# Kernel optimization log

Hardware: AMD Instinct MI355X
Metric: run time of the kernel (lower is better)

The kernel has to match this reference:

```python
import jax, jax.numpy as jnp
import numpy as np

NS, NC, T, NB = 32, 16, 64, 512
NSC = NS + NC


def setup_inputs() -> dict:
    key = jax.random.key(0)
    k1, k2, k3, k4, k5 = jax.random.split(key, 5)
    # SPD cost matrices so Quu is invertible (as assumed by the LQR math)
    L = jax.random.normal(k1, (NB, T, NSC, NSC), jnp.float32) * 0.1
    Q = L @ jnp.swapaxes(L, -1, -2) + jnp.eye(NSC, dtype=jnp.float32)
    p = jax.random.normal(k2, (NB, T, NSC), jnp.float32)
    x_init = jax.random.normal(k3, (NB, NS), jnp.float32)
    # stable-ish LTI dynamics
    A = 0.9 * jnp.eye(NS, dtype=jnp.float32) + 0.01 * jax.random.normal(k4, (NS, NS), jnp.float32)
    B = 0.1 * jax.random.normal(k5, (NS, NC), jnp.float32)
    dt = jnp.float32(0.1)
    return {"x_init": x_init, "Q": Q, "p": p, "A": A, "B": B, "dt": dt}


def _lqr(x_init, Q, p, A, B):
    ns, nc = A.shape[0], B.shape[1]
    nb, Th = Q.shape[0], Q.shape[1]
    dtype = Q.dtype

    # --- nominal rollout with zero control: x_{t+1} = A x_t ---
    def roll(x, _):
        return x @ A.T, x
    _, cx = jax.lax.scan(roll, x_init, None, length=Th)   # [T,B,ns] states x_0..x_{T-1}
    cu = jnp.zeros((Th, nb, nc), dtype)                    # current_u = 0
    xu = jnp.concatenate([cx, cu], -1)                     # [T,B,nsc]

    Qs = jnp.swapaxes(Q, 0, 1)                             # [T,B,nsc,nsc]
    ps = jnp.swapaxes(p, 0, 1)                             # [T,B,nsc]
    p_new = jnp.einsum('tbij,tbj->tbi', Qs, xu) + ps       # [T,B,nsc]

    F = jnp.concatenate([A, B], axis=1)                    # [ns, nsc]

    # --- backward Riccati recursion (V=v=0 at t=T-1 makes Qt=Q[T-1]) ---
    def bwd(carry, inp):
        V, v = carry                                       # [B,ns,ns], [B,ns]
        Qt_in, qt_in = inp
        Qt = Qt_in + jnp.einsum('si,bst,tj->bij', F, V, F)
        qt = qt_in + v @ F                                 # F^T v
        Qxx, Qxu = Qt[:, :ns, :ns], Qt[:, :ns, ns:]
        Qux, Quu = Qt[:, ns:, :ns], Qt[:, ns:, ns:]
        qx, qu = qt[:, :ns], qt[:, ns:]
        Quu_inv = jnp.linalg.pinv(Quu)
        Kt = -Quu_inv @ Qux                                # [B,nc,ns]
        kt = -jnp.einsum('bij,bj->bi', Quu_inv, qu)        # [B,nc]
        KtT = jnp.swapaxes(Kt, -1, -2)
        Vn = Qxx + Qxu @ Kt + KtT @ Qux + KtT @ Quu @ Kt
        vn = (qx + jnp.einsum('bij,bj->bi', Qxu, kt)
              + jnp.einsum('bij,bj->bi', KtT, qu)
              + jnp.einsum('bij,bj->bi', KtT @ Quu, kt))
        return (Vn, vn), (Kt, kt)

    V0 = jnp.zeros((nb, ns, ns), dtype)
    v0 = jnp.zeros((nb, ns), dtype)
    _, (Ks, ks) = jax.lax.scan(bwd, (V0, v0), (Qs, p_new), reverse=True)

    # --- forward rollout with feedback policy ---
    def fwd(carry, inp):
        xt, cost = carry
        Kt, kt, cxt, cut, Qt, pt = inp
        dut = jnp.einsum('bij,bj->bi', Kt, xt - cxt) + kt
        ut = dut + cut
        xut = jnp.concatenate([xt, ut], -1)
        cost = cost + 0.5 * jnp.einsum('bi,bij,bj->b', xut, Qt, xut) + (xut * pt).sum(-1)
        xn = xt @ A.T + ut @ B.T
        return (xn, cost), (xt, ut)

    (_, cost), (xs, us) = jax.lax.scan(
        fwd, (x_init, jnp.zeros(nb, dtype)), (Ks, ks, cx, cu, Qs, ps))
    x = jnp.swapaxes(xs, 0, 1)   # [B,T,ns]  (states x_0..x_{T-1}, matching x[...,:-1,:])
    u = jnp.swapaxes(us, 0, 1)   # [B,T,nc]
    return x, u, cost


def reference(x_init, Q, p, A, B, dt):
    # dt only matters for nonlinear relinearization; with constant LTI (A,B) it is unused.
    return _lqr(x_init, Q, p, A, B)
```

## Files before the change

kernel.cpp:

```cpp
#include <hip/hip_runtime.h>


#define NSd 32
#define NCd 16
#define Td 64
#define NBd 512
#define NSCd 48
#define SQS 52
#define TP 40

typedef __bf16 bf16x8 __attribute__((ext_vector_type(8)));
typedef __bf16 bf16x4 __attribute__((ext_vector_type(4)));
typedef float f32x4 __attribute__((ext_vector_type(4)));

#define MFMA16(a, b, c) __builtin_amdgcn_mfma_f32_16x16x32_bf16(a, b, c, 0, 0, 0)

#define XOFF ((size_t)0)
#define UOFF ((size_t)NBd * Td * NSd)
#define COFF (UOFF + (size_t)NBd * Td * NCd)

__device__ __forceinline__ float rdl(float v, int l) {
  return __uint_as_float(__builtin_amdgcn_readlane(__float_as_uint(v), l));
}

__device__ __forceinline__ void bar_lgkm() {
  asm volatile("s_waitcnt lgkmcnt(0)\n\ts_barrier" ::: "memory");
}

union LdsU {
  struct {
    __bf16 FTh[48][TP], FTl[48][TP];
    __bf16 Vh[32][TP], Vl[32][TP];
    __bf16 WTh[48][TP], WTl[48][TP];
    __bf16 Xh[32][TP], Xl[32][TP];
    __bf16 KTh[32][TP], KTl[32][TP];
    float Quu[16][17];
    float Qd[3][16][17];
    float qt[48];
    float vv[32];
  } bw;
  struct {
    float K2T[2][16 * 36];
    float kv2[2][16];
    float d[32];
    float xs[32];
    float uu[16];
  } fw;
};

#define SQSTORE(i, v)                            \
  do {                                           \
    int _r = (i) / 12, _c = (i) - _r * 12;       \
    *(float4*)&sQ[_r * SQS + _c * 4] = (v);      \
  } while (0)

__global__ __launch_bounds__(256, 2) void lqr_kernel(
    const float* __restrict__ x_init, const float* __restrict__ Qg,
    const float* __restrict__ pg, const float* __restrict__ Ag,
    const float* __restrict__ Bg, float* __restrict__ out,
    float* __restrict__ wsK, float* __restrict__ wskv) {
  const int b = blockIdx.x;
  const int tid = threadIdx.x;
  const int w = tid >> 6;
  const int lane = tid & 63;
  const int fn = lane & 15;
  const int quad = lane >> 4;
  const int k0 = quad * 8;

  __shared__ __attribute__((aligned(16))) float sQ[48 * SQS];
  __shared__ __attribute__((aligned(16))) float scx[Td][NSd];
  __shared__ __attribute__((aligned(16))) float sFf[NSd][SQS];
  __shared__ __attribute__((aligned(16))) LdsU U;
  __shared__ float scostp[4];

  for (int idx = tid; idx < 1536; idx += 256) {
    int i = idx / 48, j = idx - i * 48;
    sFf[i][j] = (j < 32) ? Ag[i * 32 + j] : Bg[i * 16 + (j - 32)];
  }
  for (int idx = tid; idx < 1536; idx += 256) {
    int a = idx >> 5, k = idx & 31;
    float f = (a < 32) ? Ag[k * 32 + a] : Bg[k * 16 + (a - 32)];
    __bf16 h = (__bf16)f;
    U.bw.FTh[a][k] = h;
    U.bw.FTl[a][k] = (__bf16)(f - (float)h);
  }
  for (int idx = tid; idx < 1024; idx += 256) {
    int r = idx >> 5, c = idx & 31;
    __bf16 z = (__bf16)0.f;
    U.bw.Vh[r][c] = z; U.bw.Vl[r][c] = z;
    U.bw.Xh[r][c] = z; U.bw.Xl[r][c] = z;
    U.bw.KTh[r][c] = z; U.bw.KTl[r][c] = z;
  }
  if (tid < 32) {
    scx[0][tid] = x_init[b * 32 + tid];
    U.bw.vv[tid] = 0.f;
  }
  {
    const float4* src = (const float4*)(Qg + ((size_t)b * Td + 63) * 2304);
    float4 v0 = src[tid];
    float4 v1 = src[tid + 256];
    SQSTORE(tid, v0);
    SQSTORE(tid + 256, v1);
    if (tid < 64) {
      float4 v2 = src[tid + 512];
      SQSTORE(tid + 512, v2);
    }
  }
  float ppf = 0.f;
  if (w == 3 && lane < 48) ppf = pg[((size_t)b * Td + 63) * 48 + lane];
  __syncthreads();

  if (w == 0) {
    for (int t2 = 0; t2 < Td - 1; ++t2) {
      if (lane < 32) {
        float acc = 0.f;
#pragma unroll
        for (int j = 0; j < 32; j += 4) {
          float4 a4 = *(const float4*)&sFf[lane][j];
          acc += a4.x * scx[t2][j] + a4.y * scx[t2][j + 1] +
                 a4.z * scx[t2][j + 2] + a4.w * scx[t2][j + 3];
        }
        scx[t2 + 1][lane] = acc;
      }
    }
  }
  __syncthreads();

  float cAcc = 0.f;
  float dAcc = 0.f;

  for (int t = Td - 1; t >= 0; --t) {
    float4 pf0, pf1, pf2;
    float ppfn;
    if (t > 0) {
      if (w < 3) {
        const float4* src = (const float4*)(Qg + ((size_t)b * Td + (t - 1)) * 2304);
        pf0 = src[tid];
        pf1 = src[tid + 192];
        pf2 = src[tid + 384];
      } else if (lane < 48) {
        ppfn = pg[((size_t)b * Td + t - 1) * 48 + lane];
      }
    }

    if (w < 3) {
      const int I = w;
      bf16x8 aH = *(const bf16x8*)&U.bw.FTh[16 * I + fn][k0];
      bf16x8 aL = *(const bf16x8*)&U.bw.FTl[16 * I + fn][k0];
#pragma unroll
      for (int J = 0; J < 2; ++J) {
        bf16x8 bH = *(const bf16x8*)&U.bw.Vh[16 * J + fn][k0];
        bf16x8 bL = *(const bf16x8*)&U.bw.Vl[16 * J + fn][k0];
        f32x4 acc = {0.f, 0.f, 0.f, 0.f};
        acc = MFMA16(aL, bH, acc);
        acc = MFMA16(aH, bL, acc);
        acc = MFMA16(aH, bH, acc);
#pragma unroll
        for (int r = 0; r < 4; ++r) {
          float v = acc[r];
          __bf16 h = (__bf16)v;
          U.bw.WTh[16 * I + 4 * quad + r][16 * J + fn] = h;
          U.bw.WTl[16 * I + 4 * quad + r][16 * J + fn] = (__bf16)(v - (float)h);
        }
      }
      bf16x8 wH = *(const bf16x8*)&U.bw.WTh[16 * I + fn][k0];
      bf16x8 wL = *(const bf16x8*)&U.bw.WTl[16 * I + fn][k0];
      if (I == 2) {
        bf16x8 bH = *(const bf16x8*)&U.bw.FTh[32 + fn][k0];
        bf16x8 bL = *(const bf16x8*)&U.bw.FTl[32 + fn][k0];
        f32x4 acc;
#pragma unroll
        for (int r = 0; r < 4; ++r)
          acc[r] = sQ[(32 + 4 * quad + r) * SQS + 32 + fn];
        acc = MFMA16(wL, bH, acc);
        acc = MFMA16(wH, bL, acc);
        acc = MFMA16(wH, bH, acc);
#pragma unroll
        for (int r = 0; r < 4; ++r) U.bw.Quu[4 * quad + r][fn] = acc[r];
      } else {
        {
          bf16x8 bH = *(const bf16x8*)&U.bw.FTh[16 * I + fn][k0];
          bf16x8 bL = *(const bf16x8*)&U.bw.FTl[16 * I + fn][k0];
          f32x4 acc;
#pragma unroll
          for (int r = 0; r < 4; ++r)
            acc[r] = sQ[(16 * I + 4 * quad + r) * SQS + 16 * I + fn];
          acc = MFMA16(wL, bH, acc);
          acc = MFMA16(wH, bL, acc);
          acc = MFMA16(wH, bH, acc);
#pragma unroll
          for (int r = 0; r < 4; ++r) U.bw.Qd[I * 2][4 * quad + r][fn] = acc[r];
        }
        if (I == 0) {
          bf16x8 bH = *(const bf16x8*)&U.bw.FTh[16 + fn][k0];
          bf16x8 bL = *(const bf16x8*)&U.bw.FTl[16 + fn][k0];
          f32x4 acc;
#pragma unroll
          for (int r = 0; r < 4; ++r)
            acc[r] = sQ[(4 * quad + r) * SQS + 16 + fn];
          acc = MFMA16(wL, bH, acc);
          acc = MFMA16(wH, bL, acc);
          acc = MFMA16(wH, bH, acc);
#pragma unroll
          for (int r = 0; r < 4; ++r) U.bw.Qd[1][4 * quad + r][fn] = acc[r];
        }
        {
          bf16x8 bH = *(const bf16x8*)&U.bw.FTh[32 + fn][k0];
          bf16x8 bL = *(const bf16x8*)&U.bw.FTl[32 + fn][k0];
          f32x4 acc;
#pragma unroll
          for (int r = 0; r < 4; ++r)
            acc[r] = sQ[(16 * I + 4 * quad + r) * SQS + 32 + fn];
          acc = MFMA16(wL, bH, acc);
          acc = MFMA16(wH, bL, acc);
          acc = MFMA16(wH, bH, acc);
#pragma unroll
          for (int r = 0; r < 4; ++r) {
            float v = acc[r];
            __bf16 h = (__bf16)v;
            U.bw.Xh[16 * I + 4 * quad + r][fn] = h;
            U.bw.Xl[16 * I + 4 * quad + r][fn] = (__bf16)(v - (float)h);
          }
        }
      }
    } else if (lane < 48) {
      float acc1 = ppf;
#pragma unroll
      for (int k = 0; k < 32; ++k) acc1 += sQ[k * SQS + lane] * scx[t][k];
      if (lane < 32) cAcc += 0.5f * scx[t][lane] * (acc1 + ppf);
      float acc = acc1;
#pragma unroll
      for (int k = 0; k < 32; ++k) acc += U.bw.vv[k] * sFf[k][lane];
      U.bw.qt[lane] = acc;
    }
    bar_lgkm();

    if (t > 0) {
      if (w < 3) {
        SQSTORE(tid, pf0);
        SQSTORE(tid + 192, pf1);
        SQSTORE(tid + 384, pf2);
      } else if (lane < 48) {
        ppf = ppfn;
      }
    }
    if (w == 3) {
      float rhs[16];
      if (lane < 32) {
        bf16x8 xh0 = *(const bf16x8*)&U.bw.Xh[lane][0];
        bf16x8 xh1 = *(const bf16x8*)&U.bw.Xh[lane][8];
        bf16x8 xl0 = *(const bf16x8*)&U.bw.Xl[lane][0];
        bf16x8 xl1 = *(const bf16x8*)&U.bw.Xl[lane][8];
#pragma unroll
        for (int i = 0; i < 8; ++i) {
          rhs[i] = (float)xh0[i] + (float)xl0[i];
          rhs[8 + i] = (float)xh1[i] + (float)xl1[i];
        }
      } else {
#pragma unroll
        for (int i = 0; i < 16; ++i) rhs[i] = U.bw.qt[32 + i];
      }
      float quu[16];
#pragma unroll
      for (int i = 0; i < 16; ++i) quu[i] = U.bw.Quu[i][fn];
#pragma unroll
      for (int r = 0; r < 15; ++r) {
        float inv = __builtin_amdgcn_rcpf(rdl(quu[r], r));
#pragma unroll
        for (int i = r + 1; i < 16; ++i) {
          float m = rdl(quu[i], r) * inv;
          rhs[i] -= m * rhs[r];
          quu[i] -= m * quu[r];
        }
      }
      float xx[16];
#pragma unroll
      for (int r = 15; r >= 0; --r) {
        float s = rhs[r];
#pragma unroll
        for (int c = r + 1; c < 16; ++c) s -= rdl(quu[r], c) * xx[c];
        xx[r] = s * __builtin_amdgcn_rcpf(rdl(quu[r], r));
      }
      if (lane < 32) {
        bf16x8 h0, l0, h1, l1;
#pragma unroll
        for (int u = 0; u < 8; ++u) {
          float kv = -xx[u];
          __bf16 hh = (__bf16)kv;
          h0[u] = hh; l0[u] = (__bf16)(kv - (float)hh);
          float kv2 = -xx[8 + u];
          __bf16 hh2 = (__bf16)kv2;
          h1[u] = hh2; l1[u] = (__bf16)(kv2 - (float)hh2);
        }
        *(bf16x8*)&U.bw.KTh[lane][0] = h0;
        *(bf16x8*)&U.bw.KTh[lane][8] = h1;
        *(bf16x8*)&U.bw.KTl[lane][0] = l0;
        *(bf16x8*)&U.bw.KTl[lane][8] = l1;
        float4* dst = (float4*)(wsK + (((size_t)b * Td + t) * 32 + lane) * 16);
        float4 v0 = {-xx[0], -xx[1], -xx[2], -xx[3]};
        float4 v1 = {-xx[4], -xx[5], -xx[6], -xx[7]};
        float4 v2 = {-xx[8], -xx[9], -xx[10], -xx[11]};
        float4 v3 = {-xx[12], -xx[13], -xx[14], -xx[15]};
        dst[0] = v0; dst[1] = v1; dst[2] = v2; dst[3] = v3;
      } else if (lane == 32) {
        float4* dst = (float4*)(wskv + ((size_t)b * Td + t) * 16);
        float4 v0 = {-xx[0], -xx[1], -xx[2], -xx[3]};
        float4 v1 = {-xx[4], -xx[5], -xx[6], -xx[7]};
        float4 v2 = {-xx[8], -xx[9], -xx[10], -xx[11]};
        float4 v3 = {-xx[12], -xx[13], -xx[14], -xx[15]};
        dst[0] = v0; dst[1] = v1; dst[2] = v2; dst[3] = v3;
        float s = 0.f;
#pragma unroll
        for (int i = 0; i < 16; ++i) s += U.bw.qt[32 + i] * xx[i];
        dAcc -= 0.5f * s;
      }
      {
        float acc = 0.f;
        bf16x8 xh0, xh1, xl0, xl1;
        if (lane < 32) {
          xh0 = *(const bf16x8*)&U.bw.Xh[lane][0];
          xh1 = *(const bf16x8*)&U.bw.Xh[lane][8];
          xl0 = *(const bf16x8*)&U.bw.Xl[lane][0];
          xl1 = *(const bf16x8*)&U.bw.Xl[lane][8];
          acc = U.bw.qt[lane];
        }
#pragma unroll
        for (int u = 0; u < 8; ++u) {
          float kt0 = -rdl(xx[u], 32);
          float kt1 = -rdl(xx[8 + u], 32);
          if (lane < 32) {
            acc += ((float)xh0[u] + (float)xl0[u]) * kt0;
            acc += ((float)xh1[u] + (float)xl1[u]) * kt1;
          }
        }
        if (lane < 32) U.bw.vv[lane] = acc;
      }
      {
        bf16x8 aH = *(const bf16x8*)&U.bw.Xh[fn][k0];
        bf16x8 aL = *(const bf16x8*)&U.bw.Xl[fn][k0];
        bf16x8 bH = *(const bf16x8*)&U.bw.KTh[fn][k0];
        bf16x8 bL = *(const bf16x8*)&U.bw.KTl[fn][k0];
        f32x4 acc;
#pragma unroll
        for (int r = 0; r < 4; ++r) acc[r] = U.bw.Qd[0][4 * quad + r][fn];
        acc = MFMA16(aL, bH, acc);
        acc = MFMA16(aH, bL, acc);
        acc = MFMA16(aH, bH, acc);
#pragma unroll
        for (int r = 0; r < 4; ++r) {
          float v = acc[r];
          __bf16 h = (__bf16)v;
          U.bw.Vh[4 * quad + r][fn] = h;
          U.bw.Vl[4 * quad + r][fn] = (__bf16)(v - (float)h);
        }
      }
      {
        bf16x8 aH = *(const bf16x8*)&U.bw.Xh[16 + fn][k0];
        bf16x8 aL = *(const bf16x8*)&U.bw.Xl[16 + fn][k0];
        bf16x8 bH = *(const bf16x8*)&U.bw.KTh[16 + fn][k0];
        bf16x8 bL = *(const bf16x8*)&U.bw.KTl[16 + fn][k0];
        f32x4 acc;
#pragma unroll
        for (int r = 0; r < 4; ++r) acc[r] = U.bw.Qd[2][4 * quad + r][fn];
        acc = MFMA16(aL, bH, acc);
        acc = MFMA16(aH, bL, acc);
        acc = MFMA16(aH, bH, acc);
#pragma unroll
        for (int r = 0; r < 4; ++r) {
          float v = acc[r];
          __bf16 h = (__bf16)v;
          U.bw.Vh[16 + 4 * quad + r][16 + fn] = h;
          U.bw.Vl[16 + 4 * quad + r][16 + fn] = (__bf16)(v - (float)h);
        }
      }
      {
        bf16x8 aH = *(const bf16x8*)&U.bw.Xh[fn][k0];
        bf16x8 aL = *(const bf16x8*)&U.bw.Xl[fn][k0];
        bf16x8 bH = *(const bf16x8*)&U.bw.KTh[16 + fn][k0];
        bf16x8 bL = *(const bf16x8*)&U.bw.KTl[16 + fn][k0];
        f32x4 acc;
#pragma unroll
        for (int r = 0; r < 4; ++r) acc[r] = U.bw.Qd[1][4 * quad + r][fn];
        acc = MFMA16(aL, bH, acc);
        acc = MFMA16(aH, bL, acc);
        acc = MFMA16(aH, bH, acc);
        bf16x4 th, tl;
#pragma unroll
        for (int r = 0; r < 4; ++r) {
          float v = acc[r];
          __bf16 h = (__bf16)v;
          __bf16 l = (__bf16)(v - (float)h);
          U.bw.Vh[4 * quad + r][16 + fn] = h;
          U.bw.Vl[4 * quad + r][16 + fn] = l;
          th[r] = h; tl[r] = l;
        }
        *(bf16x4*)&U.bw.Vh[16 + fn][4 * quad] = th;
        *(bf16x4*)&U.bw.Vl[16 + fn][4 * quad] = tl;
      }
    }
    bar_lgkm();
  }

  if (w == 3) {
    float rv = (lane < 32) ? cAcc : (lane == 32 ? dAcc : 0.f);
    rv += __shfl_down(rv, 32);
    rv += __shfl_down(rv, 16);
    rv += __shfl_down(rv, 8);
    rv += __shfl_down(rv, 4);
    rv += __shfl_down(rv, 2);
    rv += __shfl_down(rv, 1);
    if (lane == 0) scostp[0] = rv;
  }
  __syncthreads();

  if (w == 0) {
    {
      const float4* src = (const float4*)(wsK + ((size_t)b * Td) * 512);
      float4 ka = src[lane * 2], kb = src[lane * 2 + 1];
      int jj = lane >> 1, ib = (lane & 1) * 8;
      float* kt2 = U.fw.K2T[0];
      kt2[(ib + 0) * 36 + jj] = ka.x; kt2[(ib + 1) * 36 + jj] = ka.y;
      kt2[(ib + 2) * 36 + jj] = ka.z; kt2[(ib + 3) * 36 + jj] = ka.w;
      kt2[(ib + 4) * 36 + jj] = kb.x; kt2[(ib + 5) * 36 + jj] = kb.y;
      kt2[(ib + 6) * 36 + jj] = kb.z; kt2[(ib + 7) * 36 + jj] = kb.w;
      if (lane < 16) U.fw.kv2[0][lane] = wskv[(size_t)b * Td * 16 + lane];
    }
    float xr = (lane < 32) ? scx[0][lane] : 0.f;
    for (int t = 0; t < Td; ++t) {
      const int cur = t & 1, nxt = cur ^ 1;
      float4 pa, pb;
      float pk;
      if (t < Td - 1) {
        const float4* src = (const float4*)(wsK + ((size_t)b * Td + t + 1) * 512);
        pa = src[lane * 2];
        pb = src[lane * 2 + 1];
        if (lane < 16) pk = wskv[((size_t)b * Td + t + 1) * 16 + lane];
      }
      if (lane < 32) {
        U.fw.d[lane] = xr - scx[t][lane];
        U.fw.xs[lane] = xr;
        out[XOFF + ((size_t)b * Td + t) * 32 + lane] = xr;
      }
      if (lane < 16) {
        float uv = U.fw.kv2[cur][lane];
        const float* kr = &U.fw.K2T[cur][lane * 36];
#pragma unroll
        for (int j4 = 0; j4 < 8; ++j4) {
          float4 kk = *(const float4*)&kr[j4 * 4];
          float4 dd = *(const float4*)&U.fw.d[j4 * 4];
          uv += kk.x * dd.x + kk.y * dd.y + kk.z * dd.z + kk.w * dd.w;
        }
        U.fw.uu[lane] = uv;
        out[UOFF + ((size_t)b * Td + t) * 16 + lane] = uv;
      }
      if (lane < 32) {
        float acc = 0.f;
#pragma unroll
        for (int j4 = 0; j4 < 8; ++j4) {
          float4 ff = *(const float4*)&sFf[lane][j4 * 4];
          float4 xv = *(const float4*)&U.fw.xs[j4 * 4];
          acc += ff.x * xv.x + ff.y * xv.y + ff.z * xv.z + ff.w * xv.w;
        }
#pragma unroll
        for (int j4 = 0; j4 < 4; ++j4) {
          float4 ff = *(const float4*)&sFf[lane][32 + j4 * 4];
          float4 uv = *(const float4*)&U.fw.uu[j4 * 4];
          acc += ff.x * uv.x + ff.y * uv.y + ff.z * uv.z + ff.w * uv.w;
        }
        xr = acc;
      }
      if (t < Td - 1) {
        int jj = lane >> 1, ib = (lane & 1) * 8;
        float* kt2 = U.fw.K2T[nxt];
        kt2[(ib + 0) * 36 + jj] = pa.x; kt2[(ib + 1) * 36 + jj] = pa.y;
        kt2[(ib + 2) * 36 + jj] = pa.z; kt2[(ib + 3) * 36 + jj] = pa.w;
        kt2[(ib + 4) * 36 + jj] = pb.x; kt2[(ib + 5) * 36 + jj] = pb.y;
        kt2[(ib + 6) * 36 + jj] = pb.z; kt2[(ib + 7) * 36 + jj] = pb.w;
        if (lane < 16) U.fw.kv2[nxt][lane] = pk;
      }
    }
    if (lane == 0) out[COFF + b] = scostp[0];
  }
}

extern "C" void kernel_launch(void* const* d_in, const int* in_sizes, int n_in,
                              void* d_out, int out_size, void* d_ws, size_t ws_size,
                              hipStream_t stream) {
  const float* x_init = (const float*)d_in[0];
  const float* Qg = (const float*)d_in[1];
  const float* pg = (const float*)d_in[2];
  const float* Ag = (const float*)d_in[3];
  const float* Bg = (const float*)d_in[4];
  float* out = (float*)d_out;
  float* wsK = (float*)d_ws;
  float* wskv = wsK + (size_t)NBd * Td * NSd * NCd;
  lqr_kernel<<<NBd, 256, 0, stream>>>(x_init, Qg, pg, Ag, Bg, out, wsK, wskv);
}
```

Before: 636.2 us.

## Split V update into precomputed F^T-products to shorten wave-3 critical path

Instead of forming V = Qxx + Qxu K + ... on wave 3 after the solve, the waves 0-2 now precompute F^T·Qxx-style terms (S1) and F^T·Qxu (S2) while wave 3 solves for K. The next step's W = F^T V is then assembled as S1 + S2·K^T, removing the serial V-update MFMAs from wave 3's path. The change also stores Quu and Qd transposed for vectorized float4 reads, and caches pivot reciprocals in the triangular solve. It adds extra MFMA work and LDS arrays, and slightly reorders rounding in the split-bf16 arithmetic.

```diff
diff --git a/kernel.cpp b/kernel.cpp
--- a/kernel.cpp
+++ b/kernel.cpp
@@ -5,9 +5,9 @@
 #define NCd 16
 #define Td 64
 #define NBd 512
-#define NSCd 48
 #define SQS 52
 #define TP 40
+#define FP 20
 
 typedef __bf16 bf16x8 __attribute__((ext_vector_type(8)));
 typedef __bf16 bf16x4 __attribute__((ext_vector_type(4)));
@@ -27,25 +27,30 @@
   asm volatile("s_waitcnt lgkmcnt(0)\n\ts_barrier" ::: "memory");
 }
 
+struct BW {
+  __bf16 FTh[48][TP], FTl[48][TP];
+  __bf16 WTh[48][TP], WTl[48][TP];
+  __bf16 Xh[32][TP], Xl[32][TP];
+  __bf16 KTh[32][TP], KTl[32][TP];
+  __bf16 XTh[16][TP], XTl[16][TP];
+  __bf16 S2h[48][TP], S2l[48][TP];
+  float S1T[6][16][FP];
+  float QdT[3][16][FP];
+  float Qd1R[16][FP];
+  float QuuT[16][FP];
+  float qt[48];
+  float vv[32];
+};
+struct FW {
+  float K2T[2][16 * 36];
+  float kv2[2][16];
+  float d[32];
+  float xs[32];
+  float uu[16];
+};
 union LdsU {
-  struct {
-    __bf16 FTh[48][TP], FTl[48][TP];
-    __bf16 Vh[32][TP], Vl[32][TP];
-    __bf16 WTh[48][TP], WTl[48][TP];
-    __bf16 Xh[32][TP], Xl[32][TP];
-    __bf16 KTh[32][TP], KTl[32][TP];
-    float Quu[16][17];
-    float Qd[3][16][17];
-    float qt[48];
-    float vv[32];
-  } bw;
-  struct {
-    float K2T[2][16 * 36];
-    float kv2[2][16];
-    float d[32];
-    float xs[32];
-    float uu[16];
-  } fw;
+  BW bw;
+  FW fw;
 };
 
 #define SQSTORE(i, v)                            \
@@ -71,7 +76,7 @@
   __shared__ __attribute__((aligned(16))) float scx[Td][NSd];
   __shared__ __attribute__((aligned(16))) float sFf[NSd][SQS];
   __shared__ __attribute__((aligned(16))) LdsU U;
-  __shared__ float scostp[4];
+  __shared__ float scostp[1];
 
   for (int idx = tid; idx < 1536; idx += 256) {
     int i = idx / 48, j = idx - i * 48;
@@ -84,13 +89,17 @@
     U.bw.FTh[a][k] = h;
     U.bw.FTl[a][k] = (__bf16)(f - (float)h);
   }
-  for (int idx = tid; idx < 1024; idx += 256) {
+  for (int idx = tid; idx < 1536; idx += 256) {
     int r = idx >> 5, c = idx & 31;
     __bf16 z = (__bf16)0.f;
-    U.bw.Vh[r][c] = z; U.bw.Vl[r][c] = z;
-    U.bw.Xh[r][c] = z; U.bw.Xl[r][c] = z;
-    U.bw.KTh[r][c] = z; U.bw.KTl[r][c] = z;
-  }
+    U.bw.S2h[r][c] = z;
+    U.bw.S2l[r][c] = z;
+    if (r < 32) {
+      U.bw.KTh[r][c] = z;
+      U.bw.KTl[r][c] = z;
+    }
+  }
+  for (int idx = tid; idx < 6 * 16 * FP; idx += 256) ((float*)U.bw.S1T)[idx] = 0.f;
   if (tid < 32) {
     scx[0][tid] = x_init[b * 32 + tid];
     U.bw.vv[tid] = 0.f;
@@ -145,22 +154,25 @@
 
     if (w < 3) {
       const int I = w;
-      bf16x8 aH = *(const bf16x8*)&U.bw.FTh[16 * I + fn][k0];
-      bf16x8 aL = *(const bf16x8*)&U.bw.FTl[16 * I + fn][k0];
-#pragma unroll
-      for (int J = 0; J < 2; ++J) {
-        bf16x8 bH = *(const bf16x8*)&U.bw.Vh[16 * J + fn][k0];
-        bf16x8 bL = *(const bf16x8*)&U.bw.Vl[16 * J + fn][k0];
-        f32x4 acc = {0.f, 0.f, 0.f, 0.f};
-        acc = MFMA16(aL, bH, acc);
-        acc = MFMA16(aH, bL, acc);
-        acc = MFMA16(aH, bH, acc);
-#pragma unroll
-        for (int r = 0; r < 4; ++r) {
-          float v = acc[r];
-          __bf16 h = (__bf16)v;
-          U.bw.WTh[16 * I + 4 * quad + r][16 * J + fn] = h;
-          U.bw.WTl[16 * I + 4 * quad + r][16 * J + fn] = (__bf16)(v - (float)h);
+      {
+        bf16x8 aH = *(const bf16x8*)&U.bw.S2h[16 * I + fn][k0];
+        bf16x8 aL = *(const bf16x8*)&U.bw.S2l[16 * I + fn][k0];
+#pragma unroll
+        for (int J = 0; J < 2; ++J) {
+          bf16x8 bH = *(const bf16x8*)&U.bw.KTh[16 * J + fn][k0];
+          bf16x8 bL = *(const bf16x8*)&U.bw.KTl[16 * J + fn][k0];
+          float4 s1 = *(const float4*)&U.bw.S1T[I * 2 + J][fn][4 * quad];
+          f32x4 acc = {s1.x, s1.y, s1.z, s1.w};
+          acc = MFMA16(aL, bH, acc);
+          acc = MFMA16(aH, bL, acc);
+          acc = MFMA16(aH, bH, acc);
+#pragma unroll
+          for (int r = 0; r < 4; ++r) {
+            float v = acc[r];
+            __bf16 h = (__bf16)v;
+            U.bw.WTh[16 * I + 4 * quad + r][16 * J + fn] = h;
+            U.bw.WTl[16 * I + 4 * quad + r][16 * J + fn] = (__bf16)(v - (float)h);
+          }
         }
       }
       bf16x8 wH = *(const bf16x8*)&U.bw.WTh[16 * I + fn][k0];
@@ -175,8 +187,8 @@
         acc = MFMA16(wL, bH, acc);
         acc = MFMA16(wH, bL, acc);
         acc = MFMA16(wH, bH, acc);
-#pragma unroll
-        for (int r = 0; r < 4; ++r) U.bw.Quu[4 * quad + r][fn] = acc[r];
+        float4 st = {acc[0], acc[1], acc[2], acc[3]};
+        *(float4*)&U.bw.QuuT[fn][4 * quad] = st;
       } else {
         {
           bf16x8 bH = *(const bf16x8*)&U.bw.FTh[16 * I + fn][k0];
@@ -188,8 +200,8 @@
           acc = MFMA16(wL, bH, acc);
           acc = MFMA16(wH, bL, acc);
           acc = MFMA16(wH, bH, acc);
-#pragma unroll
-          for (int r = 0; r < 4; ++r) U.bw.Qd[I * 2][4 * quad + r][fn] = acc[r];
+          float4 st = {acc[0], acc[1], acc[2], acc[3]};
+          *(float4*)&U.bw.QdT[I * 2][fn][4 * quad] = st;
         }
         if (I == 0) {
           bf16x8 bH = *(const bf16x8*)&U.bw.FTh[16 + fn][k0];
@@ -201,8 +213,10 @@
           acc = MFMA16(wL, bH, acc);
           acc = MFMA16(wH, bL, acc);
           acc = MFMA16(wH, bH, acc);
-#pragma unroll
-          for (int r = 0; r < 4; ++r) U.bw.Qd[1][4 * quad + r][fn] = acc[r];
+          float4 st = {acc[0], acc[1], acc[2], acc[3]};
+          *(float4*)&U.bw.QdT[1][fn][4 * quad] = st;
+#pragma unroll
+          for (int r = 0; r < 4; ++r) U.bw.Qd1R[4 * quad + r][fn] = acc[r];
         }
         {
           bf16x8 bH = *(const bf16x8*)&U.bw.FTh[32 + fn][k0];
@@ -214,13 +228,19 @@
           acc = MFMA16(wL, bH, acc);
           acc = MFMA16(wH, bL, acc);
           acc = MFMA16(wH, bH, acc);
+          bf16x4 th, tl;
 #pragma unroll
           for (int r = 0; r < 4; ++r) {
             float v = acc[r];
             __bf16 h = (__bf16)v;
+            __bf16 l = (__bf16)(v - (float)h);
             U.bw.Xh[16 * I + 4 * quad + r][fn] = h;
-            U.bw.Xl[16 * I + 4 * quad + r][fn] = (__bf16)(v - (float)h);
+            U.bw.Xl[16 * I + 4 * quad + r][fn] = l;
+            th[r] = h;
+            tl[r] = l;
           }
+          *(bf16x4*)&U.bw.XTh[fn][16 * I + 4 * quad] = th;
+          *(bf16x4*)&U.bw.XTl[fn][16 * I + 4 * quad] = tl;
         }
       }
     } else if (lane < 48) {
@@ -244,6 +264,51 @@
         ppf = ppfn;
       }
     }
+    if (w < 3 && t > 0) {
+      const int I = w;
+      bf16x8 aH = *(const bf16x8*)&U.bw.FTh[16 * I + fn][k0];
+      bf16x8 aL = *(const bf16x8*)&U.bw.FTl[16 * I + fn][k0];
+#pragma unroll
+      for (int J = 0; J < 2; ++J) {
+        const float* bsrc;
+        if (J == 0)
+          bsrc = (quad < 2) ? &U.bw.QdT[0][fn][0] : &U.bw.Qd1R[fn][0];
+        else
+          bsrc = (quad < 2) ? &U.bw.QdT[1][fn][0] : &U.bw.QdT[2][fn][0];
+        const int off = (quad & 1) * 8;
+        float4 c0 = *(const float4*)&bsrc[off];
+        float4 c1 = *(const float4*)&bsrc[off + 4];
+        float bf[8] = {c0.x, c0.y, c0.z, c0.w, c1.x, c1.y, c1.z, c1.w};
+        bf16x8 bH, bL;
+#pragma unroll
+        for (int j = 0; j < 8; ++j) {
+          __bf16 h = (__bf16)bf[j];
+          bH[j] = h;
+          bL[j] = (__bf16)(bf[j] - (float)h);
+        }
+        f32x4 acc = {0.f, 0.f, 0.f, 0.f};
+        acc = MFMA16(aL, bH, acc);
+        acc = MFMA16(aH, bL, acc);
+        acc = MFMA16(aH, bH, acc);
+        float4 st = {acc[0], acc[1], acc[2], acc[3]};
+        *(float4*)&U.bw.S1T[I * 2 + J][fn][4 * quad] = st;
+      }
+      {
+        bf16x8 bH = *(const bf16x8*)&U.bw.XTh[fn][k0];
+        bf16x8 bL = *(const bf16x8*)&U.bw.XTl[fn][k0];
+        f32x4 acc = {0.f, 0.f, 0.f, 0.f};
+        acc = MFMA16(aL, bH, acc);
+        acc = MFMA16(aH, bL, acc);
+        acc = MFMA16(aH, bH, acc);
+#pragma unroll
+        for (int r = 0; r < 4; ++r) {
+          float v = acc[r];
+          __bf16 h = (__bf16)v;
+          U.bw.S2h[16 * I + 4 * quad + r][fn] = h;
+          U.bw.S2l[16 * I + 4 * quad + r][fn] = (__bf16)(v - (float)h);
+        }
+      }
+    }
     if (w == 3) {
       float rhs[16];
       if (lane < 32) {
@@ -261,25 +326,29 @@
         for (int i = 0; i < 16; ++i) rhs[i] = U.bw.qt[32 + i];
       }
       float quu[16];
-#pragma unroll
-      for (int i = 0; i < 16; ++i) quu[i] = U.bw.Quu[i][fn];
+      *(float4*)&quu[0] = *(const float4*)&U.bw.QuuT[fn][0];
+      *(float4*)&quu[4] = *(const float4*)&U.bw.QuuT[fn][4];
+      *(float4*)&quu[8] = *(const float4*)&U.bw.QuuT[fn][8];
+      *(float4*)&quu[12] = *(const float4*)&U.bw.QuuT[fn][12];
+      float inv[16];
 #pragma unroll
       for (int r = 0; r < 15; ++r) {
-        float inv = __builtin_amdgcn_rcpf(rdl(quu[r], r));
+        inv[r] = __builtin_amdgcn_rcpf(rdl(quu[r], r));
 #pragma unroll
         for (int i = r + 1; i < 16; ++i) {
-          float m = rdl(quu[i], r) * inv;
+          float m = rdl(quu[i], r) * inv[r];
           rhs[i] -= m * rhs[r];
           quu[i] -= m * quu[r];
         }
       }
+      inv[15] = __builtin_amdgcn_rcpf(rdl(quu[15], 15));
       float xx[16];
 #pragma unroll
       for (int r = 15; r >= 0; --r) {
         float s = rhs[r];
 #pragma unroll
         for (int c = r + 1; c < 16; ++c) s -= rdl(quu[r], c) * xx[c];
-        xx[r] = s * __builtin_amdgcn_rcpf(rdl(quu[r], r));
+        xx[r] = s * inv[r];
       }
       if (lane < 32) {
         bf16x8 h0, l0, h1, l1;
@@ -287,10 +356,12 @@
         for (int u = 0; u < 8; ++u) {
           float kv = -xx[u];
           __bf16 hh = (__bf16)kv;
-          h0[u] = hh; l0[u] = (__bf16)(kv - (float)hh);
+          h0[u] = hh;
+          l0[u] = (__bf16)(kv - (float)hh);
           float kv2 = -xx[8 + u];
           __bf16 hh2 = (__bf16)kv2;
-          h1[u] = hh2; l1[u] = (__bf16)(kv2 - (float)hh2);
+          h1[u] = hh2;
+          l1[u] = (__bf16)(kv2 - (float)hh2);
         }
         *(bf16x8*)&U.bw.KTh[lane][0] = h0;
         *(bf16x8*)&U.bw.KTh[lane][8] = h1;
@@ -335,68 +406,6 @@
         }
         if (lane < 32) U.bw.vv[lane] = acc;
       }
-      {
-        bf16x8 aH = *(const bf16x8*)&U.bw.Xh[fn][k0];
-        bf16x8 aL = *(const bf16x8*)&U.bw.Xl[fn][k0];
-        bf16x8 bH = *(const bf16x8*)&U.bw.KTh[fn][k0];
-        bf16x8 bL = *(const bf16x8*)&U.bw.KTl[fn][k0];
-        f32x4 acc;
-#pragma unroll
-        for (int r = 0; r < 4; ++r) acc[r] = U.bw.Qd[0][4 * quad + r][fn];
-        acc = MFMA16(aL, bH, acc);
-        acc = MFMA16(aH, bL, acc);
-        acc = MFMA16(aH, bH, acc);
-#pragma unroll
-        for (int r = 0; r < 4; ++r) {
-          float v = acc[r];
-          __bf16 h = (__bf16)v;
-          U.bw.Vh[4 * quad + r][fn] = h;
-          U.bw.Vl[4 * quad + r][fn] = (__bf16)(v - (float)h);
-        }
-      }
-      {
-        bf16x8 aH = *(const bf16x8*)&U.bw.Xh[16 + fn][k0];
-        bf16x8 aL = *(const bf16x8*)&U.bw.Xl[16 + fn][k0];
-        bf16x8 bH = *(const bf16x8*)&U.bw.KTh[16 + fn][k0];
-        bf16x8 bL = *(const bf16x8*)&U.bw.KTl[16 + fn][k0];
-        f32x4 acc;
-#pragma unroll
-        for (int r = 0; r < 4; ++r) acc[r] = U.bw.Qd[2][4 * quad + r][fn];
-        acc = MFMA16(aL, bH, acc);
-        acc = MFMA16(aH, bL, acc);
-        acc = MFMA16(aH, bH, acc);
-#pragma unroll
-        for (int r = 0; r < 4; ++r) {
-          float v = acc[r];
-          __bf16 h = (__bf16)v;
-          U.bw.Vh[16 + 4 * quad + r][16 + fn] = h;
-          U.bw.Vl[16 + 4 * quad + r][16 + fn] = (__bf16)(v - (float)h);
-        }
-      }
-      {
-        bf16x8 aH = *(const bf16x8*)&U.bw.Xh[fn][k0];
-        bf16x8 aL = *(const bf16x8*)&U.bw.Xl[fn][k0];
-        bf16x8 bH = *(const bf16x8*)&U.bw.KTh[16 + fn][k0];
-        bf16x8 bL = *(const bf16x8*)&U.bw.KTl[16 + fn][k0];
-        f32x4 acc;
-#pragma unroll
-        for (int r = 0; r < 4; ++r) acc[r] = U.bw.Qd[1][4 * quad + r][fn];
-        acc = MFMA16(aL, bH, acc);
-        acc = MFMA16(aH, bL, acc);
-        acc = MFMA16(aH, bH, acc);
-        bf16x4 th, tl;
-#pragma unroll
-        for (int r = 0; r < 4; ++r) {
-          float v = acc[r];
-          __bf16 h = (__bf16)v;
-          __bf16 l = (__bf16)(v - (float)h);
-          U.bw.Vh[4 * quad + r][16 + fn] = h;
-          U.bw.Vl[4 * quad + r][16 + fn] = l;
-          th[r] = h; tl[r] = l;
-        }
-        *(bf16x4*)&U.bw.Vh[16 + fn][4 * quad] = th;
-        *(bf16x4*)&U.bw.Vl[16 + fn][4 * quad] = tl;
-      }
     }
     bar_lgkm();
   }
```

New measurement: 620.8 us. 1.02x faster.
